# Performance work log

Measured on AMD Instinct MI355X. Metric: run time of the kernel, lower is better.

The kernel has to match this reference:

```python
import jax, jax.numpy as jnp
import numpy as np

EPS = 1e-5
NUM_HEADS = 16

def layernorm(x, g, b):
    mu = jnp.mean(x, axis=-1, keepdims=True)
    var = jnp.mean(jnp.square(x - mu), axis=-1, keepdims=True)
    return (x - mu) * jax.lax.rsqrt(var + EPS) * g + b

def setup_inputs() -> dict:
    key = jax.random.key(0)
    ks = jax.random.split(key, 5)
    B, N, C = 2, 2048, 1024
    s_in = 1.0 / np.sqrt(C)
    return {
        "x": jax.random.normal(ks[0], (B, N, C), jnp.float32),
        "ln1_g": jnp.ones((C,), jnp.float32),
        "ln1_b": jnp.zeros((C,), jnp.float32),
        "w_qk": jax.random.normal(ks[1], (C, 2 * C), jnp.float32) * s_in,
        "w_v": jax.random.normal(ks[2], (C, C), jnp.float32) * s_in,
        "ln2_g": jnp.ones((C,), jnp.float32),
        "ln2_b": jnp.zeros((C,), jnp.float32),
        "w_proj": jax.random.normal(ks[3], (C, C), jnp.float32) * s_in,
        "b_proj": jnp.zeros((C,), jnp.float32),
    }

def reference(x, ln1_g, ln1_b, w_qk, w_v, ln2_g, ln2_b, w_proj, b_proj):
    B, N, C = x.shape
    H = NUM_HEADS
    hd = C // H
    scale = hd ** (-0.5)
    xn = layernorm(x, ln1_g, ln1_b)
    # qk: [B,N,2C] -> q,k each [B,H,N,hd]
    qk = (xn @ w_qk).reshape(B, N, 2, H, hd).transpose(2, 0, 3, 1, 4)
    q, k = qk[0], qk[1]
    v = (xn @ w_v).reshape(B, N, H, hd).transpose(0, 2, 1, 3)  # [B,H,N,hd]
    attn = jnp.einsum("bhqd,bhkd->bhqk", q, k) * scale
    attn = jax.nn.softmax(attn, axis=-1)
    out = jnp.einsum("bhqk,bhkd->bhqd", attn, v)  # [B,H,N,hd]
    out = out.transpose(0, 2, 1, 3).reshape(B, N, C)
    out = layernorm(out, ln2_g, ln2_b)
    return out @ w_proj + b_proj
```

## Files before the change

### kernel.cpp

```cpp
#include <hip/hip_runtime.h>
#include <hip/hip_bf16.h>


typedef __attribute__((ext_vector_type(8))) short short8;
typedef __attribute__((ext_vector_type(4))) short short4v;
typedef __attribute__((ext_vector_type(4))) float float4v;
typedef __attribute__((ext_vector_type(4))) unsigned uint4v;

__device__ __forceinline__ unsigned short f2bf(float f) {
    unsigned u = __builtin_bit_cast(unsigned, f);
    return (unsigned short)((u + 0x7FFFu + ((u >> 16) & 1u)) >> 16);
}
__device__ __forceinline__ unsigned cvtpk(float lo, float hi) {
    unsigned r;
    asm("v_cvt_pk_bf16_f32 %0, %1, %2" : "=v"(r) : "v"(lo), "v"(hi));
    return r;
}
__device__ __forceinline__ void gll16(const unsigned short* g, unsigned short* l) {
    __builtin_amdgcn_global_load_lds(
        (const __attribute__((address_space(1))) unsigned int*)g,
        (__attribute__((address_space(3))) unsigned int*)l, 16, 0, 0);
}

__global__ __launch_bounds__(256) void prep(
    const float* __restrict__ x, const float* __restrict__ g1, const float* __restrict__ b1,
    const float* __restrict__ w_qk, const float* __restrict__ w_v,
    const float* __restrict__ w_proj, const float* __restrict__ g2,
    const float* __restrict__ b2,
    unsigned short* __restrict__ xn, unsigned short* __restrict__ wqkvT,
    unsigned short* __restrict__ wgT, float* __restrict__ u, float* __restrict__ w0) {
    __shared__ float sh[32 * 33];
    const int bid = blockIdx.x, tid = threadIdx.x;
    if (bid < 4096) {
        const float4 v = reinterpret_cast<const float4*>(x + (size_t)bid * 1024)[tid];
        float s  = v.x + v.y + v.z + v.w;
        float sq = v.x * v.x + v.y * v.y + v.z * v.z + v.w * v.w;
#pragma unroll
        for (int off = 32; off >= 1; off >>= 1) {
            s  += __shfl_xor(s, off, 64);
            sq += __shfl_xor(sq, off, 64);
        }
        const int w = tid >> 6, lane = tid & 63;
        if (lane == 0) { sh[w] = s; sh[4 + w] = sq; }
        __syncthreads();
        s  = sh[0] + sh[1] + sh[2] + sh[3];
        sq = sh[4] + sh[5] + sh[6] + sh[7];
        const float mu = s * (1.f / 1024.f);
        const float rstd = rsqrtf(sq * (1.f / 1024.f) - mu * mu + 1e-5f);
        const float4 gv = reinterpret_cast<const float4*>(g1)[tid];
        const float4 bv = reinterpret_cast<const float4*>(b1)[tid];
        ushort4 o;
        o.x = f2bf((v.x - mu) * rstd * gv.x + bv.x);
        o.y = f2bf((v.y - mu) * rstd * gv.y + bv.y);
        o.z = f2bf((v.z - mu) * rstd * gv.z + bv.z);
        o.w = f2bf((v.w - mu) * rstd * gv.w + bv.w);
        *reinterpret_cast<ushort4*>(&xn[(size_t)bid * 1024 + tid * 4]) = o;
    } else {
        const float* in; unsigned short* out; int Cc, bx, by; bool doU = false;
        if (bid < 6144)      { int t = bid - 4096; in = w_qk;   out = wqkvT;               Cc = 2048; bx = t & 63; by = t >> 6; }
        else if (bid < 7168) { int t = bid - 6144; in = w_v;    out = wqkvT + 2048 * 1024; Cc = 1024; bx = t & 31; by = t >> 5; }
        else                 { int t = bid - 7168; in = w_proj; out = wgT; doU = true;     Cc = 1024; bx = t & 31; by = t >> 5; }
        const int c0 = bx * 32, r0 = by * 32;
        const int tx = tid & 31, ty = tid >> 5;
#pragma unroll
        for (int i = 0; i < 32; i += 8)
            sh[(ty + i) * 33 + tx] = in[(size_t)(r0 + ty + i) * Cc + c0 + tx];
        __syncthreads();
        const float scale = doU ? g2[r0 + tx] : 1.f;
        const float b2v   = doU ? b2[r0 + tx] : 0.f;
#pragma unroll
        for (int i = 0; i < 32; i += 8) {
            const float raw = sh[tx * 33 + ty + i];
            const float sc  = raw * scale;
            out[(size_t)(c0 + ty + i) * 1024 + r0 + tx] = f2bf(sc);
            if (doU) {
                float pu = sc, pw = raw * b2v;
#pragma unroll
                for (int off = 1; off <= 16; off <<= 1) {
                    pu += __shfl_xor(pu, off, 64);
                    pw += __shfl_xor(pw, off, 64);
                }
                if (tx == 0) {
                    atomicAdd(&u[c0 + ty + i], pu);
                    atomicAdd(&w0[c0 + ty + i], pw);
                }
            }
        }
    }
}

__global__ __launch_bounds__(512, 2) void gemm_qkv(const unsigned short* __restrict__ A,
                                                   const unsigned short* __restrict__ Bt,
                                                   unsigned short* __restrict__ qb,
                                                   unsigned short* __restrict__ kb,
                                                   unsigned short* __restrict__ vT) {
    __shared__ unsigned short As[2 * 128 * 64];
    __shared__ unsigned short Bs[2 * 192 * 64];
    const int tid = threadIdx.x, lane = tid & 63, w = tid >> 6;
    const int wm = (w >> 2) * 64, wn = (w & 3) * 48;
    const int quad = lane >> 4, l16 = lane & 15;
    const int ls = lane >> 3, sg = lane & 7;
    const int m0 = blockIdx.y * 128, n0 = blockIdx.x * 192;

    float4v acc[4][3];
#pragma unroll
    for (int mi = 0; mi < 4; mi++)
#pragma unroll
        for (int ni = 0; ni < 3; ni++) acc[mi][ni] = float4v{0.f, 0.f, 0.f, 0.f};

    const int g = (sg ^ ls) * 8;
#pragma unroll
    for (int i = 0; i < 2; i++)
        gll16(&A[(size_t)(m0 + w * 16 + i * 8 + ls) * 1024 + g], &As[(w * 16 + i * 8) * 64]);
#pragma unroll
    for (int i = 0; i < 3; i++)
        gll16(&Bt[(size_t)(n0 + w * 24 + i * 8 + ls) * 1024 + g], &Bs[(w * 24 + i * 8) * 64]);

#pragma unroll 1
    for (int s = 0; s < 16; s++) {
        __syncthreads();
        if (s + 1 < 16) {
            const int k0 = (s + 1) << 6;
            unsigned short* Ad = As + (((s + 1) & 1) << 13);
            unsigned short* Bd = Bs + (((s + 1) & 1) * 12288);
#pragma unroll
            for (int i = 0; i < 2; i++)
                gll16(&A[(size_t)(m0 + w * 16 + i * 8 + ls) * 1024 + k0 + g],
                      &Ad[(w * 16 + i * 8) * 64]);
#pragma unroll
            for (int i = 0; i < 3; i++)
                gll16(&Bt[(size_t)(n0 + w * 24 + i * 8 + ls) * 1024 + k0 + g],
                      &Bd[(w * 24 + i * 8) * 64]);
        }
        const unsigned short* Ac = As + ((s & 1) << 13);
        const unsigned short* Bc = Bs + ((s & 1) * 12288);
#pragma unroll
        for (int ks = 0; ks < 2; ks++) {
            short8 af[4], bfr[3];
#pragma unroll
            for (int mi = 0; mi < 4; mi++) {
                const int r = wm + mi * 16 + l16;
                af[mi] = *reinterpret_cast<const short8*>(
                    &Ac[r * 64 + ((ks * 4 + quad) ^ (r & 7)) * 8]);
            }
#pragma unroll
            for (int ni = 0; ni < 3; ni++) {
                const int r = wn + ni * 16 + l16;
                bfr[ni] = *reinterpret_cast<const short8*>(
                    &Bc[r * 64 + ((ks * 4 + quad) ^ (r & 7)) * 8]);
            }
#pragma unroll
            for (int mi = 0; mi < 4; mi++)
#pragma unroll
                for (int ni = 0; ni < 3; ni++)
                    acc[mi][ni] = __builtin_amdgcn_mfma_f32_16x16x32_bf16(
                        af[mi], bfr[ni], acc[mi][ni], 0, 0, 0);
        }
    }

    const float QSCALE = 0.125f * 1.4426950408889634f;
#pragma unroll
    for (int mi = 0; mi < 4; mi++) {
        const int row0 = m0 + wm + mi * 16 + quad * 4;
        const int b = row0 >> 11, nq = row0 & 2047;
#pragma unroll
        for (int ni = 0; ni < 3; ni++) {
            const int col = n0 + wn + ni * 16 + l16;
            if (col < 1024) {
                const int h = col >> 6, d = col & 63;
#pragma unroll
                for (int r = 0; r < 4; r++)
                    qb[(((size_t)b * 16 + h) * 2048 + nq + r) * 64 + d] =
                        f2bf(acc[mi][ni][r] * QSCALE);
            } else if (col < 2048) {
                const int c = col - 1024, h = c >> 6, d = c & 63;
#pragma unroll
                for (int r = 0; r < 4; r++)
                    kb[(((size_t)b * 16 + h) * 2048 + nq + r) * 64 + d] = f2bf(acc[mi][ni][r]);
            } else {
                const int c = col - 2048, h = c >> 6, d = c & 63;
                const short4v sv = {(short)f2bf(acc[mi][ni][0]), (short)f2bf(acc[mi][ni][1]),
                                    (short)f2bf(acc[mi][ni][2]), (short)f2bf(acc[mi][ni][3])};
                *reinterpret_cast<short4v*>(
                    &vT[(((size_t)b * 16 + h) * 64 + d) * 2048 + nq]) = sv;
            }
        }
    }
}

__global__ __launch_bounds__(512, 4) void flash_attn(const unsigned short* __restrict__ qbuf,
                                                     const unsigned short* __restrict__ kb,
                                                     const unsigned short* __restrict__ vT,
                                                     unsigned short* __restrict__ attn,
                                                     float2* __restrict__ part) {
    __shared__ __align__(16) unsigned short KV[4][64 * 64];
    __shared__ float lsh[4][2][64];
    const int tid = threadIdx.x, lane = tid & 63, w = tid >> 6;
    const int wq = w & 3, kh = w >> 2;
    const int quad = lane >> 4, l16 = lane & 15;
    const int ls = lane >> 3, sg = lane & 7;
    const int bh = blockIdx.x, q0 = blockIdx.y * 128;
    const size_t nbase = (size_t)bh * 2048;

    const int pr = w * 8 + ls;
    const int srow = (pr & 32) | ((pr & 12) << 1) | ((pr & 16) >> 2) | (pr & 3);
    const int sgran = (sg ^ ls) << 3;

    short8 bq[2][2];
#pragma unroll
    for (int q2 = 0; q2 < 2; q2++)
#pragma unroll
        for (int ks = 0; ks < 2; ks++)
            bq[q2][ks] = *reinterpret_cast<const short8*>(
                &qbuf[(nbase + q0 + wq * 32 + q2 * 16 + l16) * 64 + ks * 32 + quad * 8]);

    float l_part[2] = {0.f, 0.f};
    float4v o_acc[2][4];
#pragma unroll
    for (int q2 = 0; q2 < 2; q2++)
#pragma unroll
        for (int db = 0; db < 4; db++) o_acc[q2][db] = float4v{0.f, 0.f, 0.f, 0.f};

    gll16(&kb[(nbase + srow) * 64 + sgran], &KV[0][w * 8 * 64]);
    gll16(&vT[((size_t)bh * 64 + w * 8 + ls) * 2048 + sgran], &KV[2][w * 8 * 64]);

#pragma unroll 1
    for (int s = 0; s < 32; s++) {
        __syncthreads();
        if (s + 1 < 32) {
            const int ktn = (s + 1) << 6, buf = (s + 1) & 1;
            gll16(&kb[(nbase + ktn + srow) * 64 + sgran], &KV[buf][w * 8 * 64]);
            gll16(&vT[((size_t)bh * 64 + w * 8 + ls) * 2048 + ktn + sgran],
                  &KV[2 + buf][w * 8 * 64]);
        }
        const unsigned short* Kc = KV[s & 1];
        const unsigned short* Vc = KV[2 + (s & 1)];

        short8 kf[2][2];
#pragma unroll
        for (int ks = 0; ks < 2; ks++)
#pragma unroll
            for (int cc = 0; cc < 2; cc++) {
                const int r = kh * 32 + cc * 16 + l16;
                kf[ks][cc] = *reinterpret_cast<const short8*>(
                    &Kc[r * 64 + ((ks * 4 + quad) ^ (r & 7)) * 8]);
            }
        short8 va[4];
#pragma unroll
        for (int db = 0; db < 4; db++) {
            const int r = db * 16 + l16;
            va[db] = *reinterpret_cast<const short8*>(
                &Vc[r * 64 + ((kh * 4 + quad) ^ (r & 7)) * 8]);
        }

#pragma unroll
        for (int q2 = 0; q2 < 2; q2++) {
            float4v s_acc[2];
#pragma unroll
            for (int cc = 0; cc < 2; cc++) s_acc[cc] = float4v{0.f, 0.f, 0.f, 0.f};
            __builtin_amdgcn_s_setprio(1);
#pragma unroll
            for (int ks = 0; ks < 2; ks++)
#pragma unroll
                for (int cc = 0; cc < 2; cc++)
                    s_acc[cc] = __builtin_amdgcn_mfma_f32_16x16x32_bf16(
                        kf[ks][cc], bq[q2][ks], s_acc[cc], 0, 0, 0);
            __builtin_amdgcn_s_setprio(0);

            float ls2 = 0.f;
            float p[8];
#pragma unroll
            for (int cc = 0; cc < 2; cc++)
#pragma unroll
                for (int r = 0; r < 4; r++) {
                    const float pv = __builtin_amdgcn_exp2f(s_acc[cc][r]);
                    p[cc * 4 + r] = pv;
                    ls2 += pv;
                }
            uint4v pd;
            pd.x = cvtpk(p[0], p[1]); pd.y = cvtpk(p[2], p[3]);
            pd.z = cvtpk(p[4], p[5]); pd.w = cvtpk(p[6], p[7]);
            const short8 pb = __builtin_bit_cast(short8, pd);
            l_part[q2] += ls2;
            __builtin_amdgcn_s_setprio(1);
#pragma unroll
            for (int db = 0; db < 4; db++)
                o_acc[q2][db] = __builtin_amdgcn_mfma_f32_16x16x32_bf16(
                    va[db], pb, o_acc[q2][db], 0, 0, 0);
            __builtin_amdgcn_s_setprio(0);
        }
    }

    __syncthreads();
    float* osh = reinterpret_cast<float*>(KV);
    const int swz = (l16 & 7) << 2;
    if (kh == 1) {
#pragma unroll
        for (int q2 = 0; q2 < 2; q2++)
#pragma unroll
            for (int db = 0; db < 4; db++) {
                const int base = (wq * 32 + q2 * 16 + l16) * 64 + db * 16 + quad * 4;
                *reinterpret_cast<float4v*>(&osh[base ^ swz]) = o_acc[q2][db];
            }
        lsh[wq][0][lane] = l_part[0];
        lsh[wq][1][lane] = l_part[1];
    }
    __syncthreads();
    if (kh == 0) {
        const int b = bh >> 4, h = bh & 15;
#pragma unroll
        for (int q2 = 0; q2 < 2; q2++) {
            float lr = l_part[q2] + lsh[wq][q2][lane];
            lr += __shfl_xor(lr, 16, 64);
            lr += __shfl_xor(lr, 32, 64);
            const float inv = 1.f / lr;
            const int grow = b * 2048 + q0 + wq * 32 + q2 * 16 + l16;
            float sum = 0.f, s2 = 0.f;
#pragma unroll
            for (int db = 0; db < 4; db++) {
                const int base = (wq * 32 + q2 * 16 + l16) * 64 + db * 16 + quad * 4;
                const float4v oh = *reinterpret_cast<const float4v*>(&osh[base ^ swz]);
                const float o0 = (o_acc[q2][db][0] + oh[0]) * inv;
                const float o1 = (o_acc[q2][db][1] + oh[1]) * inv;
                const float o2 = (o_acc[q2][db][2] + oh[2]) * inv;
                const float o3 = (o_acc[q2][db][3] + oh[3]) * inv;
                const ushort4 st = {f2bf(o0), f2bf(o1), f2bf(o2), f2bf(o3)};
                *reinterpret_cast<ushort4*>(
                    &attn[(size_t)grow * 1024 + h * 64 + db * 16 + quad * 4]) = st;
                sum += (o0 + o1) + (o2 + o3);
                s2  += (o0 * o0 + o1 * o1) + (o2 * o2 + o3 * o3);
            }
            sum += __shfl_xor(sum, 16, 64); sum += __shfl_xor(sum, 32, 64);
            s2  += __shfl_xor(s2, 16, 64);  s2  += __shfl_xor(s2, 32, 64);
            if (quad == 0) part[(size_t)grow * 16 + h] = float2{sum, s2};
        }
    }
}

__global__ __launch_bounds__(256) void gemm_proj(const unsigned short* __restrict__ A,
                                                 const unsigned short* __restrict__ Bt,
                                                 const float2* __restrict__ part,
                                                 const float* __restrict__ u,
                                                 const float* __restrict__ w0,
                                                 const float* __restrict__ bias,
                                                 float* __restrict__ out) {
    __shared__ unsigned short As[2 * 128 * 64];
    __shared__ unsigned short Bs[2 * 64 * 64];
    __shared__ float2 rstat_s[128];
    const int tid = threadIdx.x, lane = tid & 63, w = tid >> 6;
    const int quad = lane >> 4, l16 = lane & 15;
    const int ls = lane >> 3, sg = lane & 7;
    const int m0 = blockIdx.y * 128, n0 = blockIdx.x * 64;
    {
        const int rloc = tid >> 1, half = tid & 1;
        const float4* p4 = reinterpret_cast<const float4*>(part);
        float s = 0.f, s2 = 0.f;
#pragma unroll
        for (int j = 0; j < 4; j++) {
            const float4 p = p4[(size_t)(m0 + rloc) * 8 + half * 4 + j];
            s += p.x + p.z; s2 += p.y + p.w;
        }
        s  += __shfl_xor(s, 1, 64);
        s2 += __shfl_xor(s2, 1, 64);
        if (!half) {
            const float mu = s * (1.f / 1024.f);
            const float rstd = rsqrtf(s2 * (1.f / 1024.f) - mu * mu + 1e-5f);
            rstat_s[rloc] = float2{rstd, mu * rstd};
        }
    }

    float4v acc[2][4];
#pragma unroll
    for (int mi = 0; mi < 2; mi++)
#pragma unroll
        for (int ni = 0; ni < 4; ni++) acc[mi][ni] = float4v{0.f, 0.f, 0.f, 0.f};

    const int g = (sg ^ ls) * 8;
#pragma unroll
    for (int i = 0; i < 4; i++)
        gll16(&A[(size_t)(m0 + w * 32 + i * 8 + ls) * 1024 + g], &As[(w * 32 + i * 8) * 64]);
#pragma unroll
    for (int i = 0; i < 2; i++)
        gll16(&Bt[(size_t)(n0 + w * 16 + i * 8 + ls) * 1024 + g], &Bs[(w * 16 + i * 8) * 64]);

#pragma unroll 1
    for (int s = 0; s < 16; s++) {
        __syncthreads();
        if (s + 1 < 16) {
            const int k0 = (s + 1) << 6;
            unsigned short* Ad = As + (((s + 1) & 1) << 13);
            unsigned short* Bd = Bs + (((s + 1) & 1) << 12);
#pragma unroll
            for (int i = 0; i < 4; i++)
                gll16(&A[(size_t)(m0 + w * 32 + i * 8 + ls) * 1024 + k0 + g],
                      &Ad[(w * 32 + i * 8) * 64]);
#pragma unroll
            for (int i = 0; i < 2; i++)
                gll16(&Bt[(size_t)(n0 + w * 16 + i * 8 + ls) * 1024 + k0 + g],
                      &Bd[(w * 16 + i * 8) * 64]);
        }
        const unsigned short* Ac = As + ((s & 1) << 13);
        const unsigned short* Bc = Bs + ((s & 1) << 12);
#pragma unroll
        for (int ks = 0; ks < 2; ks++) {
            short8 af[2], bfr[4];
#pragma unroll
            for (int mi = 0; mi < 2; mi++) {
                const int r = w * 32 + mi * 16 + l16;
                af[mi] = *reinterpret_cast<const short8*>(
                    &Ac[r * 64 + ((ks * 4 + quad) ^ (r & 7)) * 8]);
            }
#pragma unroll
            for (int ni = 0; ni < 4; ni++) {
                const int r = ni * 16 + l16;
                bfr[ni] = *reinterpret_cast<const short8*>(
                    &Bc[r * 64 + ((ks * 4 + quad) ^ (r & 7)) * 8]);
            }
#pragma unroll
            for (int mi = 0; mi < 2; mi++)
#pragma unroll
                for (int ni = 0; ni < 4; ni++)
                    acc[mi][ni] = __builtin_amdgcn_mfma_f32_16x16x32_bf16(
                        af[mi], bfr[ni], acc[mi][ni], 0, 0, 0);
        }
    }

#pragma unroll
    for (int mi = 0; mi < 2; mi++) {
        const int rl0 = w * 32 + mi * 16 + quad * 4;
        float2 rs[4];
#pragma unroll
        for (int r = 0; r < 4; r++) rs[r] = rstat_s[rl0 + r];
#pragma unroll
        for (int ni = 0; ni < 4; ni++) {
            const int col = n0 + ni * 16 + l16;
            const float uu = u[col], ww = w0[col] + bias[col];
#pragma unroll
            for (int r = 0; r < 4; r++)
                out[(size_t)(m0 + rl0 + r) * 1024 + col] =
                    fmaf(rs[r].x, acc[mi][ni][r], ww - rs[r].y * uu);
        }
    }
}

extern "C" void kernel_launch(void* const* d_in, const int* in_sizes, int n_in,
                              void* d_out, int out_size, void* d_ws, size_t ws_size,
                              hipStream_t stream) {
    const float* x      = (const float*)d_in[0];
    const float* ln1_g  = (const float*)d_in[1];
    const float* ln1_b  = (const float*)d_in[2];
    const float* w_qk   = (const float*)d_in[3];
    const float* w_v    = (const float*)d_in[4];
    const float* ln2_g  = (const float*)d_in[5];
    const float* ln2_b  = (const float*)d_in[6];
    const float* w_proj = (const float*)d_in[7];
    const float* b_proj = (const float*)d_in[8];
    float* out = (float*)d_out;

    char* ws = (char*)d_ws;
    unsigned short* xn      = (unsigned short*)(ws + 0);
    unsigned short* wqkvT   = (unsigned short*)(ws + 8388608);
    unsigned short* wgT     = (unsigned short*)(ws + 14680064);
    unsigned short* qbuf    = (unsigned short*)(ws + 16777216);
    unsigned short* kbuf    = (unsigned short*)(ws + 25165824);
    unsigned short* vTbuf   = (unsigned short*)(ws + 33554432);
    unsigned short* attn    = (unsigned short*)(ws + 41943040);
    float2*         part    = (float2*)(ws + 50331648);
    float*          u       = (float*)(ws + 50888704);
    float*          w0      = (float*)(ws + 50892800);

    hipMemsetAsync(ws + 50888704, 0, 8192, stream);
    prep<<<8192, 256, 0, stream>>>(x, ln1_g, ln1_b, w_qk, w_v, w_proj, ln2_g, ln2_b,
                                   xn, wqkvT, wgT, u, w0);
    gemm_qkv<<<dim3(16, 32), 512, 0, stream>>>(xn, wqkvT, qbuf, kbuf, vTbuf);
    flash_attn<<<dim3(32, 16), 512, 0, stream>>>(qbuf, kbuf, vTbuf, attn, part);
    gemm_proj<<<dim3(16, 32), 256, 0, stream>>>(attn, wgT, part, u, w0, b_proj, out);
}
```

Baseline: 186.8 us.

## Double KV stage depth in flash attention and use wave-per-row LayerNorm

The attention loop now loads two 64-key tiles per pipeline stage, halving the number of block barriers and iterations, at the cost of doubling shared memory for K/V buffers. The LayerNorm part of the prep kernel assigns one wave per row, so the cross-wave shared-memory reduction and barrier are removed and the prep grid shrinks. The larger LDS footprint may limit how many attention blocks fit per CU.

```diff
diff --git a/kernel.cpp b/kernel.cpp
--- a/kernel.cpp
+++ b/kernel.cpp
@@ -31,35 +31,42 @@
     unsigned short* __restrict__ wgT, float* __restrict__ u, float* __restrict__ w0) {
     __shared__ float sh[32 * 33];
     const int bid = blockIdx.x, tid = threadIdx.x;
-    if (bid < 4096) {
-        const float4 v = reinterpret_cast<const float4*>(x + (size_t)bid * 1024)[tid];
-        float s  = v.x + v.y + v.z + v.w;
-        float sq = v.x * v.x + v.y * v.y + v.z * v.z + v.w * v.w;
+    if (bid < 1024) {
+        const int lane = tid & 63;
+        const int row = bid * 4 + (tid >> 6);
+        const float4* xr = reinterpret_cast<const float4*>(x + (size_t)row * 1024);
+        const float4* G4 = reinterpret_cast<const float4*>(g1);
+        const float4* B4 = reinterpret_cast<const float4*>(b1);
+        float4 v[4];
+        float s = 0.f, sq = 0.f;
+#pragma unroll
+        for (int i = 0; i < 4; i++) {
+            v[i] = xr[i * 64 + lane];
+            s  += (v[i].x + v[i].y) + (v[i].z + v[i].w);
+            sq += (v[i].x * v[i].x + v[i].y * v[i].y) + (v[i].z * v[i].z + v[i].w * v[i].w);
+        }
 #pragma unroll
         for (int off = 32; off >= 1; off >>= 1) {
             s  += __shfl_xor(s, off, 64);
             sq += __shfl_xor(sq, off, 64);
         }
-        const int w = tid >> 6, lane = tid & 63;
-        if (lane == 0) { sh[w] = s; sh[4 + w] = sq; }
-        __syncthreads();
-        s  = sh[0] + sh[1] + sh[2] + sh[3];
-        sq = sh[4] + sh[5] + sh[6] + sh[7];
         const float mu = s * (1.f / 1024.f);
         const float rstd = rsqrtf(sq * (1.f / 1024.f) - mu * mu + 1e-5f);
-        const float4 gv = reinterpret_cast<const float4*>(g1)[tid];
-        const float4 bv = reinterpret_cast<const float4*>(b1)[tid];
-        ushort4 o;
-        o.x = f2bf((v.x - mu) * rstd * gv.x + bv.x);
-        o.y = f2bf((v.y - mu) * rstd * gv.y + bv.y);
-        o.z = f2bf((v.z - mu) * rstd * gv.z + bv.z);
-        o.w = f2bf((v.w - mu) * rstd * gv.w + bv.w);
-        *reinterpret_cast<ushort4*>(&xn[(size_t)bid * 1024 + tid * 4]) = o;
+#pragma unroll
+        for (int i = 0; i < 4; i++) {
+            const float4 gv = G4[i * 64 + lane], bv = B4[i * 64 + lane];
+            ushort4 o;
+            o.x = f2bf((v[i].x - mu) * rstd * gv.x + bv.x);
+            o.y = f2bf((v[i].y - mu) * rstd * gv.y + bv.y);
+            o.z = f2bf((v[i].z - mu) * rstd * gv.z + bv.z);
+            o.w = f2bf((v[i].w - mu) * rstd * gv.w + bv.w);
+            *reinterpret_cast<ushort4*>(&xn[(size_t)row * 1024 + i * 256 + lane * 4]) = o;
+        }
     } else {
         const float* in; unsigned short* out; int Cc, bx, by; bool doU = false;
-        if (bid < 6144)      { int t = bid - 4096; in = w_qk;   out = wqkvT;               Cc = 2048; bx = t & 63; by = t >> 6; }
-        else if (bid < 7168) { int t = bid - 6144; in = w_v;    out = wqkvT + 2048 * 1024; Cc = 1024; bx = t & 31; by = t >> 5; }
-        else                 { int t = bid - 7168; in = w_proj; out = wgT; doU = true;     Cc = 1024; bx = t & 31; by = t >> 5; }
+        if (bid < 3072)      { int t = bid - 1024; in = w_qk;   out = wqkvT;               Cc = 2048; bx = t & 63; by = t >> 6; }
+        else if (bid < 4096) { int t = bid - 3072; in = w_v;    out = wqkvT + 2048 * 1024; Cc = 1024; bx = t & 31; by = t >> 5; }
+        else                 { int t = bid - 4096; in = w_proj; out = wgT; doU = true;     Cc = 1024; bx = t & 31; by = t >> 5; }
         const int c0 = bx * 32, r0 = by * 32;
         const int tx = tid & 31, ty = tid >> 5;
 #pragma unroll
@@ -193,7 +200,8 @@
                                                      const unsigned short* __restrict__ vT,
                                                      unsigned short* __restrict__ attn,
                                                      float2* __restrict__ part) {
-    __shared__ __align__(16) unsigned short KV[4][64 * 64];
+    __shared__ __align__(16) unsigned short KB[2][2][64 * 64];
+    __shared__ __align__(16) unsigned short VB[2][2][64 * 64];
     __shared__ float lsh[4][2][64];
     const int tid = threadIdx.x, lane = tid & 63, w = tid >> 6;
     const int wq = w & 3, kh = w >> 2;
@@ -221,78 +229,86 @@
 #pragma unroll
         for (int db = 0; db < 4; db++) o_acc[q2][db] = float4v{0.f, 0.f, 0.f, 0.f};
 
-    gll16(&kb[(nbase + srow) * 64 + sgran], &KV[0][w * 8 * 64]);
-    gll16(&vT[((size_t)bh * 64 + w * 8 + ls) * 2048 + sgran], &KV[2][w * 8 * 64]);
+#define FSTAGE(t, buf)                                                                  \
+    _Pragma("unroll")                                                                   \
+    for (int t2 = 0; t2 < 2; t2++) {                                                    \
+        gll16(&kb[(nbase + (t) * 128 + t2 * 64 + srow) * 64 + sgran],                   \
+              &KB[buf][t2][w * 8 * 64]);                                                \
+        gll16(&vT[((size_t)bh * 64 + w * 8 + ls) * 2048 + (t) * 128 + t2 * 64 + sgran], \
+              &VB[buf][t2][w * 8 * 64]);                                                \
+    }
+
+    FSTAGE(0, 0);
 
 #pragma unroll 1
-    for (int s = 0; s < 32; s++) {
+    for (int s = 0; s < 16; s++) {
         __syncthreads();
-        if (s + 1 < 32) {
-            const int ktn = (s + 1) << 6, buf = (s + 1) & 1;
-            gll16(&kb[(nbase + ktn + srow) * 64 + sgran], &KV[buf][w * 8 * 64]);
-            gll16(&vT[((size_t)bh * 64 + w * 8 + ls) * 2048 + ktn + sgran],
-                  &KV[2 + buf][w * 8 * 64]);
-        }
-        const unsigned short* Kc = KV[s & 1];
-        const unsigned short* Vc = KV[2 + (s & 1)];
-
-        short8 kf[2][2];
-#pragma unroll
-        for (int ks = 0; ks < 2; ks++)
-#pragma unroll
-            for (int cc = 0; cc < 2; cc++) {
-                const int r = kh * 32 + cc * 16 + l16;
-                kf[ks][cc] = *reinterpret_cast<const short8*>(
-                    &Kc[r * 64 + ((ks * 4 + quad) ^ (r & 7)) * 8]);
-            }
-        short8 va[4];
-#pragma unroll
-        for (int db = 0; db < 4; db++) {
-            const int r = db * 16 + l16;
-            va[db] = *reinterpret_cast<const short8*>(
-                &Vc[r * 64 + ((kh * 4 + quad) ^ (r & 7)) * 8]);
-        }
-
-#pragma unroll
-        for (int q2 = 0; q2 < 2; q2++) {
-            float4v s_acc[2];
-#pragma unroll
-            for (int cc = 0; cc < 2; cc++) s_acc[cc] = float4v{0.f, 0.f, 0.f, 0.f};
-            __builtin_amdgcn_s_setprio(1);
+        if (s + 1 < 16) FSTAGE(s + 1, (s + 1) & 1);
+
+#pragma unroll
+        for (int t2 = 0; t2 < 2; t2++) {
+            const unsigned short* Kc = KB[s & 1][t2];
+            const unsigned short* Vc = VB[s & 1][t2];
+
+            short8 kf[2][2];
 #pragma unroll
             for (int ks = 0; ks < 2; ks++)
 #pragma unroll
+                for (int cc = 0; cc < 2; cc++) {
+                    const int r = kh * 32 + cc * 16 + l16;
+                    kf[ks][cc] = *reinterpret_cast<const short8*>(
+                        &Kc[r * 64 + ((ks * 4 + quad) ^ (r & 7)) * 8]);
+                }
+            short8 va[4];
+#pragma unroll
+            for (int db = 0; db < 4; db++) {
+                const int r = db * 16 + l16;
+                va[db] = *reinterpret_cast<const short8*>(
+                    &Vc[r * 64 + ((kh * 4 + quad) ^ (r & 7)) * 8]);
+            }
+
+#pragma unroll
+            for (int q2 = 0; q2 < 2; q2++) {
+                float4v s_acc[2];
+#pragma unroll
+                for (int cc = 0; cc < 2; cc++) s_acc[cc] = float4v{0.f, 0.f, 0.f, 0.f};
+                __builtin_amdgcn_s_setprio(1);
+#pragma unroll
+                for (int ks = 0; ks < 2; ks++)
+#pragma unroll
+                    for (int cc = 0; cc < 2; cc++)
+                        s_acc[cc] = __builtin_amdgcn_mfma_f32_16x16x32_bf16(
+                            kf[ks][cc], bq[q2][ks], s_acc[cc], 0, 0, 0);
+                __builtin_amdgcn_s_setprio(0);
+
+                float ls2 = 0.f;
+                float p[8];
+#pragma unroll
                 for (int cc = 0; cc < 2; cc++)
-                    s_acc[cc] = __builtin_amdgcn_mfma_f32_16x16x32_bf16(
-                        kf[ks][cc], bq[q2][ks], s_acc[cc], 0, 0, 0);
-            __builtin_amdgcn_s_setprio(0);
-
-            float ls2 = 0.f;
-            float p[8];
-#pragma unroll
-            for (int cc = 0; cc < 2; cc++)
-#pragma unroll
-                for (int r = 0; r < 4; r++) {
-                    const float pv = __builtin_amdgcn_exp2f(s_acc[cc][r]);
-                    p[cc * 4 + r] = pv;
-                    ls2 += pv;
-                }
-            uint4v pd;
-            pd.x = cvtpk(p[0], p[1]); pd.y = cvtpk(p[2], p[3]);
-            pd.z = cvtpk(p[4], p[5]); pd.w = cvtpk(p[6], p[7]);
-            const short8 pb = __builtin_bit_cast(short8, pd);
-            l_part[q2] += ls2;
-            __builtin_amdgcn_s_setprio(1);
-#pragma unroll
-            for (int db = 0; db < 4; db++)
-                o_acc[q2][db] = __builtin_amdgcn_mfma_f32_16x16x32_bf16(
-                    va[db], pb, o_acc[q2][db], 0, 0, 0);
-            __builtin_amdgcn_s_setprio(0);
-        }
-    }
+#pragma unroll
+                    for (int r = 0; r < 4; r++) {
+                        const float pv = __builtin_amdgcn_exp2f(s_acc[cc][r]);
+                        p[cc * 4 + r] = pv;
+                        ls2 += pv;
+                    }
+                uint4v pd;
+                pd.x = cvtpk(p[0], p[1]); pd.y = cvtpk(p[2], p[3]);
+                pd.z = cvtpk(p[4], p[5]); pd.w = cvtpk(p[6], p[7]);
+                const short8 pb = __builtin_bit_cast(short8, pd);
+                l_part[q2] += ls2;
+                __builtin_amdgcn_s_setprio(1);
+#pragma unroll
+                for (int db = 0; db < 4; db++)
+                    o_acc[q2][db] = __builtin_amdgcn_mfma_f32_16x16x32_bf16(
+                        va[db], pb, o_acc[q2][db], 0, 0, 0);
+                __builtin_amdgcn_s_setprio(0);
+            }
+        }
+    }
+#undef FSTAGE
 
     __syncthreads();
-    float* osh = reinterpret_cast<float*>(KV);
+    float* osh = reinterpret_cast<float*>(KB);
     const int swz = (l16 & 7) << 2;
     if (kh == 1) {
 #pragma unroll
@@ -470,7 +486,7 @@
     float*          w0      = (float*)(ws + 50892800);
 
     hipMemsetAsync(ws + 50888704, 0, 8192, stream);
-    prep<<<8192, 256, 0, stream>>>(x, ln1_g, ln1_b, w_qk, w_v, w_proj, ln2_g, ln2_b,
+    prep<<<5120, 256, 0, stream>>>(x, ln1_g, ln1_b, w_qk, w_v, w_proj, ln2_g, ln2_b,
                                    xn, wqkvT, wgT, u, w0);
     gemm_qkv<<<dim3(16, 32), 512, 0, stream>>>(xn, wqkvT, qbuf, kbuf, vTbuf);
     flash_attn<<<dim3(32, 16), 512, 0, stream>>>(qbuf, kbuf, vTbuf, attn, part);
```

Measured after the change: 186.8 us. About the same (+0.0%).
